# Kernel optimization log

Measured on AMD Instinct MI355X. Metric: run time of the kernel, lower is better.

Reference implementation:

```python
import jax, jax.numpy as jnp
import numpy as np

WIDTH = 1024

def setup_inputs() -> dict:
    key = jax.random.key(0)
    ks = jax.random.split(key, 5)
    x = jax.random.normal(ks[0], (4, 4096, WIDTH), dtype=jnp.float32)
    # LayerNorm params
    ln_gamma = jnp.ones((WIDTH,), dtype=jnp.float32)
    ln_beta = jnp.zeros((WIDTH,), dtype=jnp.float32)
    # Linear params (torch nn.Linear init: U(-1/sqrt(fan_in), 1/sqrt(fan_in)))
    bound = 1.0 / np.sqrt(WIDTH)
    w1 = jax.random.uniform(ks[1], (WIDTH, WIDTH), jnp.float32, -bound, bound)
    b1 = jax.random.uniform(ks[2], (WIDTH,), jnp.float32, -bound, bound)
    w2 = jax.random.uniform(ks[3], (WIDTH, WIDTH), jnp.float32, -bound, bound)
    b2 = jax.random.uniform(ks[4], (WIDTH,), jnp.float32, -bound, bound)
    return {"x": x, "ln_gamma": ln_gamma, "ln_beta": ln_beta,
            "w1": w1, "b1": b1, "w2": w2, "b2": b2}

def _layernorm(x, gamma, beta, eps=1e-5):
    mu = jnp.mean(x, axis=-1, keepdims=True)
    var = jnp.mean(jnp.square(x - mu), axis=-1, keepdims=True)
    return (x - mu) * jax.lax.rsqrt(var + eps) * gamma + beta

def reference(x, ln_gamma, ln_beta, w1, b1, w2, b2):
    # Pre-norm residual MLP: x + W2 @ gelu(W1 @ LN(x) + b1) + b2
    h = _layernorm(x, ln_gamma, ln_beta)
    h = jnp.einsum('bsd,ed->bse', h, w1) + b1  # w stored as [out, in] like torch
    h = jax.nn.gelu(h, approximate=False)      # torch nn.GELU default = exact erf
    # dropout p=0.0 -> identity
    h = jnp.einsum('bsd,ed->bse', h, w2) + b2
    return x + h
```

## Files before the change

### kernel.cpp

```cpp
#include <hip/hip_runtime.h>
#include <hip/hip_bf16.h>
#include <math.h>

typedef __bf16 bf16x8 __attribute__((ext_vector_type(8)));
typedef float f32x4 __attribute__((ext_vector_type(4)));

#define GAS __attribute__((address_space(1)))
#define LAS __attribute__((address_space(3)))

static __device__ __forceinline__ void load16(const void* g, void* l) {
    __builtin_amdgcn_global_load_lds((const GAS void*)g, (LAS void*)l, 16, 0, 0);
}

struct __align__(8) bh4 { __hip_bfloat16 x, y, z, w; };

__global__ __launch_bounds__(256) void pre_kernel(
        const float* __restrict__ x, const float* __restrict__ gamma,
        const float* __restrict__ beta, const float* __restrict__ w1,
        const float* __restrict__ w2, __hip_bfloat16* __restrict__ hn,
        __hip_bfloat16* __restrict__ w1b, __hip_bfloat16* __restrict__ w2b, int nln) {
    if ((int)blockIdx.x >= nln) {
        const int i = (blockIdx.x - nln) * 256 + threadIdx.x;
        float4 a = ((const float4*)w1)[i];
        float4 b = ((const float4*)w2)[i];
        bh4 r1, r2;
        r1.x = __float2bfloat16(a.x); r1.y = __float2bfloat16(a.y);
        r1.z = __float2bfloat16(a.z); r1.w = __float2bfloat16(a.w);
        r2.x = __float2bfloat16(b.x); r2.y = __float2bfloat16(b.y);
        r2.z = __float2bfloat16(b.z); r2.w = __float2bfloat16(b.w);
        ((bh4*)w1b)[i] = r1;
        ((bh4*)w2b)[i] = r2;
        return;
    }
    const int row  = (blockIdx.x << 2) + (threadIdx.x >> 6);
    const int lane = threadIdx.x & 63;
    const float4* px = (const float4*)(x + (size_t)row * 1024);
    float4 v[4];
    float s = 0.f;
#pragma unroll
    for (int i = 0; i < 4; ++i) {
        v[i] = px[lane + (i << 6)];
        s += v[i].x + v[i].y + v[i].z + v[i].w;
    }
#pragma unroll
    for (int o = 32; o; o >>= 1) s += __shfl_xor(s, o, 64);
    const float mu = s * (1.0f / 1024.0f);
    float vs = 0.f;
#pragma unroll
    for (int i = 0; i < 4; ++i) {
        float a = v[i].x - mu, b = v[i].y - mu, c = v[i].z - mu, d = v[i].w - mu;
        vs += a * a + b * b + c * c + d * d;
    }
#pragma unroll
    for (int o = 32; o; o >>= 1) vs += __shfl_xor(vs, o, 64);
    const float rs = rsqrtf(vs * (1.0f / 1024.0f) + 1e-5f);
    const float4* pg = (const float4*)gamma;
    const float4* pb = (const float4*)beta;
    bh4* po = (bh4*)(hn + (size_t)row * 1024);
#pragma unroll
    for (int i = 0; i < 4; ++i) {
        const int idx = lane + (i << 6);
        float4 g = pg[idx], bb = pb[idx];
        bh4 r;
        r.x = __float2bfloat16((v[i].x - mu) * rs * g.x + bb.x);
        r.y = __float2bfloat16((v[i].y - mu) * rs * g.y + bb.y);
        r.z = __float2bfloat16((v[i].z - mu) * rs * g.z + bb.z);
        r.w = __float2bfloat16((v[i].w - mu) * rs * g.w + bb.w);
        po[idx] = r;
    }
}

__device__ __forceinline__ float gelu_exact(float v) {
    const float ax = fabsf(v) * 0.70710678118654752f;
    const float t  = __builtin_amdgcn_rcpf(__builtin_fmaf(0.3275911f, ax, 1.0f));
    float p = __builtin_fmaf(1.061405429f, t, -1.453152027f);
    p = __builtin_fmaf(p, t, 1.421413741f);
    p = __builtin_fmaf(p, t, -0.284496736f);
    p = __builtin_fmaf(p, t, 0.254829592f);
    p *= t;
    const float e  = __expf(-ax * ax);
    const float er = __builtin_fmaf(-p, e, 1.0f);
    return 0.5f * v * (1.0f + copysignf(er, v));
}

#define SCB() __builtin_amdgcn_sched_barrier(0)
#define BAR() do { __builtin_amdgcn_s_barrier(); SCB(); } while (0)
#define LGKM(n) do { asm volatile("s_waitcnt lgkmcnt(" #n ")" ::: "memory"); SCB(); } while (0)
#define VMW(n) do { asm volatile("s_waitcnt vmcnt(" #n ")" ::: "memory"); SCB(); } while (0)

__device__ __forceinline__ void rd4(const char* base, int stride, bf16x8 (&v)[4]) {
#pragma unroll
    for (int i = 0; i < 4; ++i) v[i] = *(const bf16x8*)(base + i * stride);
}

#define MFMA16(AF, BF) do { __builtin_amdgcn_s_setprio(1); \
    _Pragma("unroll") for (int i2 = 0; i2 < 4; ++i2) \
    _Pragma("unroll") for (int j2 = 0; j2 < 4; ++j2) \
        acc[i2][j2] = __builtin_amdgcn_mfma_f32_16x16x32_bf16(AF[i2], BF[j2], acc[i2][j2], 0, 0, 0); \
    __builtin_amdgcn_s_setprio(0); } while (0)

#define TILE128(CUR, OTH, KOFF, S1) do { \
    const char* aB_ = aBase + (CUR) * 16384; \
    const char* bB_ = bBase + (CUR) * 16384; \
    rd4(aB_ + px0, 2048, af0); SCB(); \
    rd4(bB_ + px0, 128, bf0); SCB(); \
    rd4(aB_ + px1, 2048, af1); SCB(); \
    rd4(bB_ + px1, 128, bf1); SCB(); \
    if (S1) { \
        char* dAo = dA + (OTH) * 16384; \
        char* dBo = dB + (OTH) * 16384; \
        load16(sa + (KOFF) + 64,             dAo); \
        load16(sb + (KOFF) + 64,             dBo); \
        load16(sa + (KOFF) + 64 + 32 * 1024, dAo + 4096); \
        load16(sb + (KOFF) + 64 + 32 * 1024, dBo + 4096); \
        load16(sa + (KOFF) + 64 + 64 * 1024, dAo + 8192); \
        load16(sb + (KOFF) + 64 + 64 * 1024, dBo + 8192); \
        load16(sa + (KOFF) + 64 + 96 * 1024, dAo + 12288); \
        load16(sb + (KOFF) + 64 + 96 * 1024, dBo + 12288); \
    } \
    LGKM(8); \
    MFMA16(af0, bf0); \
    LGKM(0); \
    MFMA16(af1, bf1); \
} while (0)

template <int EPI>
__global__ __launch_bounds__(256, 2) void gemm128(
        const __hip_bfloat16* __restrict__ A,
        const __hip_bfloat16* __restrict__ B,
        const float* __restrict__ bias,
        const float* __restrict__ resid,
        __hip_bfloat16* __restrict__ outb,
        float* __restrict__ outf) {
    constexpr int K = 1024, N = 1024;
    __shared__ __align__(16) char sA[32768];
    __shared__ __align__(16) char sB[32768];

    const int tid  = threadIdx.x;
    const int lane = tid & 63;
    const int w    = tid >> 6;
    const int wm   = (w >> 1) * 64;
    const int wn   = (w & 1) * 64;
    const int bm   = blockIdx.x * 128;
    const int bn   = blockIdx.y * 128;

    const int f = lane & 15;
    const int h = lane >> 4;

    const int srow = tid >> 3;
    const int lA_chunk = (tid & 7) ^ (srow & 7);
    const int lB_chunk = (tid & 7) ^ ((tid >> 5) & 7);
    const __hip_bfloat16* sa = A + (size_t)(bm + srow) * K + lA_chunk * 8;
    const __hip_bfloat16* sb = B + (size_t)(bn + srow) * K + lB_chunk * 8;
    char* dA = sA + tid * 16;
    char* dB = sB + tid * 16;

    const int pxk = (f & 7) * 16;
    const int px0 = (h * 16) ^ pxk;
    const int px1 = ((4 + h) * 16) ^ pxk;
    const char* aBase = sA + (wm + f) * 128;
    const char* bBase = sB + (wn + 4 * f) * 128;

    f32x4 acc[4][4] = {};
    bf16x8 af0[4], af1[4], bf0[4], bf1[4];

    load16(sa, dA);                 load16(sb, dB);
    load16(sa + 32 * 1024, dA + 4096); load16(sb + 32 * 1024, dB + 4096);
    load16(sa + 64 * 1024, dA + 8192); load16(sb + 64 * 1024, dB + 8192);
    load16(sa + 96 * 1024, dA + 12288); load16(sb + 96 * 1024, dB + 12288);
    VMW(0);
    BAR();

#pragma unroll 1
    for (int it = 0; it < 7; ++it) {
        const int k0 = it << 7;
        TILE128(0, 1, k0, true);
        VMW(0); BAR();
        TILE128(1, 0, k0 + 64, true);
        VMW(0); BAR();
    }
    TILE128(0, 1, 896, true);
    VMW(0); BAR();
    TILE128(1, 0, 960, false);

    const int colb = bn + wn + f * 4;
    const float4 bias4 = *(const float4*)(bias + colb);
#pragma unroll
    for (int i = 0; i < 4; ++i) {
#pragma unroll
        for (int r = 0; r < 4; ++r) {
            const size_t grow = (size_t)(bm + wm + i * 16 + h * 4 + r);
            float v0 = acc[i][0][r] + bias4.x;
            float v1 = acc[i][1][r] + bias4.y;
            float v2 = acc[i][2][r] + bias4.z;
            float v3 = acc[i][3][r] + bias4.w;
            if (EPI == 0) {
                bh4 o;
                o.x = __float2bfloat16(gelu_exact(v0));
                o.y = __float2bfloat16(gelu_exact(v1));
                o.z = __float2bfloat16(gelu_exact(v2));
                o.w = __float2bfloat16(gelu_exact(v3));
                *(bh4*)(outb + grow * N + colb) = o;
            } else {
                const float4 rs = *(const float4*)(resid + grow * N + colb);
                float4 o = {v0 + rs.x, v1 + rs.y, v2 + rs.z, v3 + rs.w};
                *(float4*)(outf + grow * N + colb) = o;
            }
        }
    }
}

extern "C" void kernel_launch(void* const* d_in, const int* in_sizes, int n_in,
                              void* d_out, int out_size, void* d_ws, size_t ws_size,
                              hipStream_t stream) {
    const float* x     = (const float*)d_in[0];
    const float* gamma = (const float*)d_in[1];
    const float* beta  = (const float*)d_in[2];
    const float* w1    = (const float*)d_in[3];
    const float* b1    = (const float*)d_in[4];
    const float* w2    = (const float*)d_in[5];
    const float* b2    = (const float*)d_in[6];
    float* out = (float*)d_out;

    const int M = in_sizes[0] / 1024;

    char* ws = (char*)d_ws;
    __hip_bfloat16* hn  = (__hip_bfloat16*)ws;
    __hip_bfloat16* h1  = (__hip_bfloat16*)(ws + (size_t)M * 2048);
    __hip_bfloat16* w1b = (__hip_bfloat16*)(ws + (size_t)M * 4096);
    __hip_bfloat16* w2b = (__hip_bfloat16*)(ws + (size_t)M * 4096 + 2097152);

    const int nln = M / 4;
    pre_kernel<<<nln + 1024, 256, 0, stream>>>(x, gamma, beta, w1, w2, hn, w1b, w2b, nln);
    gemm128<0><<<dim3(M / 128, 8), 256, 0, stream>>>(hn, w1b, b1, nullptr, h1, nullptr);
    gemm128<1><<<dim3(M / 128, 8), 256, 0, stream>>>(h1, w2b, b2, x, nullptr, out);
}
```

Measured before the change: 209.4 us.

## Fold LayerNorm affine into W1/b1 and normalize x inside first GEMM

```diff
diff --git a/kernel.cpp b/kernel.cpp
--- a/kernel.cpp
+++ b/kernel.cpp
@@ -14,26 +14,47 @@
 
 struct __align__(8) bh4 { __hip_bfloat16 x, y, z, w; };
 
-__global__ __launch_bounds__(256) void pre_kernel(
+__global__ __launch_bounds__(256) void prep_kernel(
         const float* __restrict__ x, const float* __restrict__ gamma,
         const float* __restrict__ beta, const float* __restrict__ w1,
-        const float* __restrict__ w2, __hip_bfloat16* __restrict__ hn,
-        __hip_bfloat16* __restrict__ w1b, __hip_bfloat16* __restrict__ w2b, int nln) {
-    if ((int)blockIdx.x >= nln) {
-        const int i = (blockIdx.x - nln) * 256 + threadIdx.x;
+        const float* __restrict__ w2, const float* __restrict__ b1,
+        float2* __restrict__ stats, __hip_bfloat16* __restrict__ w1g,
+        __hip_bfloat16* __restrict__ w2b, float* __restrict__ b1g, int nln) {
+    const int bid = blockIdx.x;
+    const int tid = threadIdx.x;
+    if (bid >= nln + 1024) {
+        const int e    = (bid - nln - 1024) * 32 + (tid >> 3);
+        const int part = tid & 7;
+        const float4* wrow = (const float4*)(w1 + (size_t)e * 1024 + part * 128);
+        const float4* bet  = (const float4*)(beta + part * 128);
+        float s = 0.f;
+#pragma unroll 8
+        for (int i = 0; i < 32; ++i) {
+            float4 wv = wrow[i], bv = bet[i];
+            s += wv.x * bv.x + wv.y * bv.y + wv.z * bv.z + wv.w * bv.w;
+        }
+        s += __shfl_xor(s, 1, 64);
+        s += __shfl_xor(s, 2, 64);
+        s += __shfl_xor(s, 4, 64);
+        if (part == 0) b1g[e] = b1[e] + s;
+        return;
+    }
+    if (bid >= nln) {
+        const int i = (bid - nln) * 256 + tid;
         float4 a = ((const float4*)w1)[i];
+        float4 g = ((const float4*)gamma)[i & 255];
         float4 b = ((const float4*)w2)[i];
         bh4 r1, r2;
-        r1.x = __float2bfloat16(a.x); r1.y = __float2bfloat16(a.y);
-        r1.z = __float2bfloat16(a.z); r1.w = __float2bfloat16(a.w);
+        r1.x = __float2bfloat16(a.x * g.x); r1.y = __float2bfloat16(a.y * g.y);
+        r1.z = __float2bfloat16(a.z * g.z); r1.w = __float2bfloat16(a.w * g.w);
         r2.x = __float2bfloat16(b.x); r2.y = __float2bfloat16(b.y);
         r2.z = __float2bfloat16(b.z); r2.w = __float2bfloat16(b.w);
-        ((bh4*)w1b)[i] = r1;
+        ((bh4*)w1g)[i] = r1;
         ((bh4*)w2b)[i] = r2;
         return;
     }
-    const int row  = (blockIdx.x << 2) + (threadIdx.x >> 6);
-    const int lane = threadIdx.x & 63;
+    const int row  = (bid << 2) + (tid >> 6);
+    const int lane = tid & 63;
     const float4* px = (const float4*)(x + (size_t)row * 1024);
     float4 v[4];
     float s = 0.f;
@@ -53,20 +74,11 @@
     }
 #pragma unroll
     for (int o = 32; o; o >>= 1) vs += __shfl_xor(vs, o, 64);
-    const float rs = rsqrtf(vs * (1.0f / 1024.0f) + 1e-5f);
-    const float4* pg = (const float4*)gamma;
-    const float4* pb = (const float4*)beta;
-    bh4* po = (bh4*)(hn + (size_t)row * 1024);
-#pragma unroll
-    for (int i = 0; i < 4; ++i) {
-        const int idx = lane + (i << 6);
-        float4 g = pg[idx], bb = pb[idx];
-        bh4 r;
-        r.x = __float2bfloat16((v[i].x - mu) * rs * g.x + bb.x);
-        r.y = __float2bfloat16((v[i].y - mu) * rs * g.y + bb.y);
-        r.z = __float2bfloat16((v[i].z - mu) * rs * g.z + bb.z);
-        r.w = __float2bfloat16((v[i].w - mu) * rs * g.w + bb.w);
-        po[idx] = r;
+    if (lane == 0) {
+        float2 st;
+        st.x = mu;
+        st.y = rsqrtf(vs * (1.0f / 1024.0f) + 1e-5f);
+        stats[row] = st;
     }
 }
 
@@ -99,29 +111,47 @@
         acc[i2][j2] = __builtin_amdgcn_mfma_f32_16x16x32_bf16(AF[i2], BF[j2], acc[i2][j2], 0, 0, 0); \
     __builtin_amdgcn_s_setprio(0); } while (0)
 
+#define XLOAD(KOFF) do { _Pragma("unroll") for (int q = 0; q < 4; ++q) { \
+    const float4* p_ = (const float4*)(xs + (KOFF) + q * 32768); \
+    xv[q][0] = p_[0]; xv[q][1] = p_[1]; } } while (0)
+
+#define XSTORE(OTH) do { _Pragma("unroll") for (int q = 0; q < 4; ++q) { \
+    const float mu_ = st4[q].x, rs_ = st4[q].y; \
+    const float4 a_ = xv[q][0], b_ = xv[q][1]; \
+    bf16x8 r_; \
+    r_[0] = (__bf16)((a_.x - mu_) * rs_); r_[1] = (__bf16)((a_.y - mu_) * rs_); \
+    r_[2] = (__bf16)((a_.z - mu_) * rs_); r_[3] = (__bf16)((a_.w - mu_) * rs_); \
+    r_[4] = (__bf16)((b_.x - mu_) * rs_); r_[5] = (__bf16)((b_.y - mu_) * rs_); \
+    r_[6] = (__bf16)((b_.z - mu_) * rs_); r_[7] = (__bf16)((b_.w - mu_) * rs_); \
+    *(bf16x8*)(dAw + (OTH) * 16384 + q * 4096) = r_; } } while (0)
+
 #define TILE128(CUR, OTH, KOFF, S1) do { \
     const char* aB_ = aBase + (CUR) * 16384; \
     const char* bB_ = bBase + (CUR) * 16384; \
+    if (EPI == 0 && (S1)) { XLOAD((KOFF) + 64); } \
     rd4(aB_ + px0, 2048, af0); SCB(); \
     rd4(bB_ + px0, 128, bf0); SCB(); \
     rd4(aB_ + px1, 2048, af1); SCB(); \
     rd4(bB_ + px1, 128, bf1); SCB(); \
     if (S1) { \
-        char* dAo = dA + (OTH) * 16384; \
         char* dBo = dB + (OTH) * 16384; \
-        load16(sa + (KOFF) + 64,             dAo); \
         load16(sb + (KOFF) + 64,             dBo); \
-        load16(sa + (KOFF) + 64 + 32 * 1024, dAo + 4096); \
         load16(sb + (KOFF) + 64 + 32 * 1024, dBo + 4096); \
-        load16(sa + (KOFF) + 64 + 64 * 1024, dAo + 8192); \
         load16(sb + (KOFF) + 64 + 64 * 1024, dBo + 8192); \
-        load16(sa + (KOFF) + 64 + 96 * 1024, dAo + 12288); \
         load16(sb + (KOFF) + 64 + 96 * 1024, dBo + 12288); \
+        if (EPI == 1) { \
+            char* dAo = dA + (OTH) * 16384; \
+            load16(sa + (KOFF) + 64,             dAo); \
+            load16(sa + (KOFF) + 64 + 32 * 1024, dAo + 4096); \
+            load16(sa + (KOFF) + 64 + 64 * 1024, dAo + 8192); \
+            load16(sa + (KOFF) + 64 + 96 * 1024, dAo + 12288); \
+        } \
     } \
     LGKM(8); \
     MFMA16(af0, bf0); \
     LGKM(0); \
     MFMA16(af1, bf1); \
+    if (EPI == 0 && (S1)) { VMW(4); XSTORE(OTH); LGKM(0); } \
 } while (0)
 
 template <int EPI>
@@ -131,7 +161,9 @@
         const float* __restrict__ bias,
         const float* __restrict__ resid,
         __hip_bfloat16* __restrict__ outb,
-        float* __restrict__ outf) {
+        float* __restrict__ outf,
+        const float* __restrict__ xsrc,
+        const float2* __restrict__ stats) {
     constexpr int K = 1024, N = 1024;
     __shared__ __align__(16) char sA[32768];
     __shared__ __align__(16) char sB[32768];
@@ -155,6 +187,11 @@
     char* dA = sA + tid * 16;
     char* dB = sB + tid * 16;
 
+    const float* xs = xsrc + (size_t)(bm + srow) * 1024 + (tid & 7) * 8;
+    char* dAw = sA + srow * 128 + (((tid & 7) ^ (srow & 7)) << 4);
+    float2 st4[4];
+    float4 xv[4][2];
+
     const int pxk = (f & 7) * 16;
     const int px0 = (h * 16) ^ pxk;
     const int px1 = ((4 + h) * 16) ^ pxk;
@@ -164,11 +201,23 @@
     f32x4 acc[4][4] = {};
     bf16x8 af0[4], af1[4], bf0[4], bf1[4];
 
-    load16(sa, dA);                 load16(sb, dB);
-    load16(sa + 32 * 1024, dA + 4096); load16(sb + 32 * 1024, dB + 4096);
-    load16(sa + 64 * 1024, dA + 8192); load16(sb + 64 * 1024, dB + 8192);
-    load16(sa + 96 * 1024, dA + 12288); load16(sb + 96 * 1024, dB + 12288);
-    VMW(0);
+    if (EPI == 0) {
+#pragma unroll
+        for (int q = 0; q < 4; ++q) st4[q] = stats[bm + srow + 32 * q];
+        XLOAD(0);
+        load16(sb, dB);                     load16(sb + 32 * 1024, dB + 4096);
+        load16(sb + 64 * 1024, dB + 8192);  load16(sb + 96 * 1024, dB + 12288);
+        VMW(4);
+        XSTORE(0);
+        LGKM(0);
+        VMW(0);
+    } else {
+        load16(sa, dA);                     load16(sb, dB);
+        load16(sa + 32 * 1024, dA + 4096);  load16(sb + 32 * 1024, dB + 4096);
+        load16(sa + 64 * 1024, dA + 8192);  load16(sb + 64 * 1024, dB + 8192);
+        load16(sa + 96 * 1024, dA + 12288); load16(sb + 96 * 1024, dB + 12288);
+        VMW(0);
+    }
     BAR();
 
 #pragma unroll 1
@@ -225,13 +274,17 @@
     const int M = in_sizes[0] / 1024;
 
     char* ws = (char*)d_ws;
-    __hip_bfloat16* hn  = (__hip_bfloat16*)ws;
-    __hip_bfloat16* h1  = (__hip_bfloat16*)(ws + (size_t)M * 2048);
-    __hip_bfloat16* w1b = (__hip_bfloat16*)(ws + (size_t)M * 4096);
-    __hip_bfloat16* w2b = (__hip_bfloat16*)(ws + (size_t)M * 4096 + 2097152);
+    __hip_bfloat16* h1  = (__hip_bfloat16*)ws;
+    __hip_bfloat16* w1g = (__hip_bfloat16*)(ws + (size_t)M * 2048);
+    __hip_bfloat16* w2b = (__hip_bfloat16*)(ws + (size_t)M * 2048 + 2097152);
+    float*          b1g = (float*)(ws + (size_t)M * 2048 + 4194304);
+    float2*       stats = (float2*)(ws + (size_t)M * 2048 + 4198400);
 
     const int nln = M / 4;
-    pre_kernel<<<nln + 1024, 256, 0, stream>>>(x, gamma, beta, w1, w2, hn, w1b, w2b, nln);
-    gemm128<0><<<dim3(M / 128, 8), 256, 0, stream>>>(hn, w1b, b1, nullptr, h1, nullptr);
-    gemm128<1><<<dim3(M / 128, 8), 256, 0, stream>>>(h1, w2b, b2, x, nullptr, out);
-}
+    prep_kernel<<<nln + 1024 + 32, 256, 0, stream>>>(
+        x, gamma, beta, w1, w2, b1, stats, w1g, w2b, b1g, nln);
+    gemm128<0><<<dim3(M / 128, 8), 256, 0, stream>>>(
+        (const __hip_bfloat16*)x, w1g, b1g, nullptr, h1, nullptr, x, stats);
+    gemm128<1><<<dim3(M / 128, 8), 256, 0, stream>>>(
+        h1, w2b, b2, x, nullptr, out, x, stats);
+}
```

New measurement: 235.6 us. 12.5% more time.
